# Performance work log

Hardware: AMD Instinct MI355X
Metric: run time of the kernel (lower is better)

## Reference

```python
import jax, jax.numpy as jnp
import numpy as np

D = 1024   # model dim (hard-coded in ClsNet)
H = 16     # num_heads
HD = D // H
FF = 2048  # torch TransformerEncoderLayer default dim_feedforward
B, LX, LY = 8, 512, 512
EPS = 1e-5
NEG = -1e9


def setup_inputs() -> dict:
    key = jax.random.key(0)
    ks = jax.random.split(key, 16)
    s = 0.02
    inp = {
        "x": jax.random.normal(ks[0], (B, LX, D), jnp.float32),
        "y": jax.random.normal(ks[1], (B, LY, D), jnp.float32),
        "cls": jax.random.normal(ks[2], (D,), jnp.float32) * s,
        "sep": jax.random.normal(ks[3], (D,), jnp.float32) * s,
        "px": jax.random.normal(ks[4], (D,), jnp.float32) * s,
        "py": jax.random.normal(ks[5], (D,), jnp.float32) * s,
        "Wqkv": jax.random.normal(ks[6], (3 * D, D), jnp.float32) * s,
        "bqkv": jnp.zeros((3 * D,), jnp.float32),
        "Wo": jax.random.normal(ks[7], (D, D), jnp.float32) * s,
        "bo": jnp.zeros((D,), jnp.float32),
        "W1": jax.random.normal(ks[8], (FF, D), jnp.float32) * s,
        "b1": jnp.zeros((FF,), jnp.float32),
        "W2": jax.random.normal(ks[9], (D, FF), jnp.float32) * s,
        "b2": jnp.zeros((D,), jnp.float32),
        "ln1_g": jnp.ones((D,), jnp.float32),
        "ln1_b": jnp.zeros((D,), jnp.float32),
        "ln2_g": jnp.ones((D,), jnp.float32),
        "ln2_b": jnp.zeros((D,), jnp.float32),
        "x_len": jax.random.randint(ks[10], (B,), 1, LX + 1, jnp.int32),
        "y_len": jax.random.randint(ks[11], (B,), 1, LY + 1, jnp.int32),
    }
    return inp


def _merge(x, y, cls, sep, px, py, x_len, y_len):
    # Vectorized version of ClsNet.merge: [CLS] x_i+px ... [SEP] y_i+py ... [SEP] pad...
    Bn, Lx, Dd = x.shape
    Ly = y.shape[1]
    S = Lx + Ly + 3
    pos = jnp.arange(S)[None, :]            # [1,S]
    lx = x_len[:, None]                     # [B,1]
    ly = y_len[:, None]
    is_cls = pos == 0                       # [1,S]
    is_x = (pos >= 1) & (pos <= lx)         # [B,S]
    is_sep1 = pos == lx + 1
    is_y = (pos >= lx + 2) & (pos <= lx + ly + 1)
    is_sep2 = pos == lx + ly + 2
    xi = jnp.clip(pos - 1, 0, Lx - 1)       # [1,S]
    yi = jnp.clip(pos - lx - 2, 0, Ly - 1)  # [B,S]
    xg = jnp.take_along_axis(x, xi[:, :, None], axis=1)  # [B,S,D] (broadcast batch)
    yg = jnp.take_along_axis(y, yi[:, :, None], axis=1)  # [B,S,D]
    seq = (jnp.where(is_x[..., None], xg + px, 0.0)
           + jnp.where(is_y[..., None], yg + py, 0.0)
           + is_cls[..., None] * cls
           + (is_sep1 | is_sep2)[..., None] * sep)       # [B,S,D]
    mask = is_cls | is_x | is_sep1 | is_y | is_sep2      # [B,S] True = valid token
    return seq, mask


def _ln(h, g, b):
    m = jnp.mean(h, axis=-1, keepdims=True)
    v = jnp.mean(jnp.square(h - m), axis=-1, keepdims=True)
    return (h - m) * jax.lax.rsqrt(v + EPS) * g + b


def _encoder_layer(seq, mask, Wqkv, bqkv, Wo, bo, W1, b1, W2, b2, ln1_g, ln1_b, ln2_g, ln2_b):
    Bn, S, Dd = seq.shape
    qkv = seq @ Wqkv.T + bqkv                              # [B,S,3D]
    q, k, v = jnp.split(qkv, 3, axis=-1)
    q = q.reshape(Bn, S, H, HD)
    k = k.reshape(Bn, S, H, HD)
    v = v.reshape(Bn, S, H, HD)
    bias = jnp.where(mask, 0.0, NEG)[:, None, None, :]     # padded KEYS masked out
    scores = jnp.einsum("bqhd,bkhd->bhqk", q, k) / np.sqrt(HD) + bias
    attn = jax.nn.softmax(scores, axis=-1)
    o = jnp.einsum("bhqk,bkhd->bqhd", attn, v).reshape(Bn, S, Dd)
    o = o @ Wo.T + bo
    h = _ln(seq + o, ln1_g, ln1_b)                          # post-norm (torch default)
    f = jax.nn.relu(h @ W1.T + b1) @ W2.T + b2
    return _ln(h + f, ln2_g, ln2_b)


def reference(x, y, cls, sep, px, py, Wqkv, bqkv, Wo, bo, W1, b1, W2, b2,
              ln1_g, ln1_b, ln2_g, ln2_b, x_len, y_len):
    seq, mask = _merge(x, y, cls, sep, px, py, x_len, y_len)
    out = _encoder_layer(seq, mask, Wqkv, bqkv, Wo, bo, W1, b1, W2, b2,
                         ln1_g, ln1_b, ln2_g, ln2_b)
    # torch code returns a[0] of the seq-first tensor -> the CLS position for all batches
    return out[:, 0, :]
```

## Files before the change

### kernel.cpp

```cpp
#include <hip/hip_runtime.h>
#include <hip/hip_bf16.h>

#define D_ 1024
#define H_ 16
#define FF_ 2048
#define B_ 8
#define S_ 1027
#define MPAD_ 8320
#define PSTR_ 1056
#define EPS_ 1e-5f

typedef __hip_bfloat16 bf16;
typedef unsigned short u16;
typedef unsigned int u32;
typedef __attribute__((ext_vector_type(4))) float floatx4;
typedef __bf16 bf16x8 __attribute__((ext_vector_type(8)));

__device__ __forceinline__ float2 bfpair(u32 u) {
  union { u32 u; float f; } lo, hi;
  lo.u = u << 16; hi.u = u & 0xffff0000u;
  return make_float2(lo.f, hi.f);
}

__device__ __forceinline__ u32 f2bfbits(float f) {
  union { bf16 h; u16 u; } cv; cv.h = __float2bfloat16(f); return (u32)cv.u;
}

__device__ __forceinline__ float block_sum(float x, float* red) {
  const int t = threadIdx.x;
  __syncthreads();
  red[t] = x;
  __syncthreads();
  for (int s = 128; s > 0; s >>= 1) {
    if (t < s) red[t] += red[t + s];
    __syncthreads();
  }
  return red[0];
}

__device__ __forceinline__ float block_max(float x, float* red) {
  const int t = threadIdx.x;
  __syncthreads();
  red[t] = x;
  __syncthreads();
  for (int s = 128; s > 0; s >>= 1) {
    if (t < s) red[t] = fmaxf(red[t], red[t + s]);
    __syncthreads();
  }
  return red[0];
}

__global__ void __launch_bounds__(256) build_seq_kernel(
    const float* __restrict__ x, const float* __restrict__ y,
    const float* __restrict__ cls, const float* __restrict__ sep,
    const float* __restrict__ px, const float* __restrict__ py,
    const int* __restrict__ x_len, const int* __restrict__ y_len,
    bf16* __restrict__ seq) {
  const int m = blockIdx.x, t = threadIdx.x;
  const int b = m / S_;
  const int s = m - b * S_;
  if (b >= B_) return;
  const float* src = nullptr;
  const float* add = nullptr;
  const int lx = x_len[b], ly = y_len[b];
  if (s == 0) src = cls;
  else if (s <= lx) { src = x + ((size_t)b * 512 + (s - 1)) * D_; add = px; }
  else if (s == lx + 1) src = sep;
  else if (s <= lx + ly + 1) { src = y + ((size_t)b * 512 + (s - lx - 2)) * D_; add = py; }
  else if (s == lx + ly + 2) src = sep;
  if (!src) return;
  float4 sv = ((const float4*)src)[t];
  if (add) {
    float4 av = ((const float4*)add)[t];
    sv.x += av.x; sv.y += av.y; sv.z += av.z; sv.w += av.w;
  }
  uint2 o;
  o.x = f2bfbits(sv.x) | (f2bfbits(sv.y) << 16);
  o.y = f2bfbits(sv.z) | (f2bfbits(sv.w) << 16);
  ((uint2*)(seq + (size_t)m * D_))[t] = o;
}

__global__ void __launch_bounds__(256) qproj_kernel(
    const float* __restrict__ cls, const float* __restrict__ Wqkv,
    const float* __restrict__ bqkv, float* __restrict__ q0s) {
  __shared__ float cl[D_];
  const int t = threadIdx.x;
  *(float4*)&cl[t * 4] = ((const float4*)cls)[t];
  __syncthreads();
  const int w = t >> 6, l = t & 63;
  const int r = blockIdx.x * 4 + w;
  float acc = 0.f;
#pragma unroll
  for (int ch = 0; ch < 4; ++ch) {
    float4 wv = *(const float4*)(Wqkv + (size_t)r * D_ + ch * 256 + l * 4);
    const float* c4 = &cl[ch * 256 + l * 4];
    acc += wv.x * c4[0] + wv.y * c4[1] + wv.z * c4[2] + wv.w * c4[3];
  }
#pragma unroll
  for (int off = 32; off > 0; off >>= 1) acc += __shfl_down(acc, off, 64);
  if (l == 0) q0s[r] = (acc + bqkv[r]) * 0.125f;
}

__global__ void __launch_bounds__(256) rproj_kernel(
    const float* __restrict__ Wqkv, const float* __restrict__ q0s,
    u16* __restrict__ RT_hi, u16* __restrict__ RT_lo) {
  const int h = blockIdx.y, cc = blockIdx.x, t = threadIdx.x;
  __shared__ float qs[64];
  if (t < 64) qs[t] = q0s[h * 64 + t];
  __syncthreads();
  const int c = cc * 256 + t;
  const float* Wk = Wqkv + (size_t)(D_ + h * 64) * D_ + c;
  float acc = 0.f;
#pragma unroll 8
  for (int e = 0; e < 64; ++e) acc += Wk[(size_t)e * D_] * qs[e];
  const u32 hb = f2bfbits(acc);
  union { u32 u; float f; } hv; hv.u = hb << 16;
  RT_hi[h * D_ + c] = (u16)hb;
  RT_lo[h * D_ + c] = (u16)f2bfbits(acc - hv.f);
}

__global__ void __launch_bounds__(256) scores_kernel(
    const bf16* __restrict__ seq, const u16* __restrict__ RT_hi,
    const u16* __restrict__ RT_lo, const int* __restrict__ x_len,
    const int* __restrict__ y_len, float* __restrict__ S) {
  const int m0 = blockIdx.x * 64;
  bool valid = false;
#pragma unroll
  for (int b = 0; b < B_; ++b) {
    int rs = b * S_, re = rs + x_len[b] + y_len[b] + 3;
    if (m0 < re && m0 + 64 > rs) valid = true;
  }
  if (!valid) return;
  const int t = threadIdx.x;
  const int w = t >> 6, lane = t & 63, lane16 = lane & 15, quad = lane >> 4;
  const int row = m0 + w * 16 + lane16;
  const u16* arow = (const u16*)seq + (size_t)row * D_ + quad * 8;
  const u16* bh = RT_hi + lane16 * D_ + quad * 8;
  const u16* bl = RT_lo + lane16 * D_ + quad * 8;
  floatx4 acc = {};
#pragma unroll 4
  for (int kt = 0; kt < 32; ++kt) {
    bf16x8 a  = *(const bf16x8*)(arow + kt * 32);
    bf16x8 vh = *(const bf16x8*)(bh + kt * 32);
    bf16x8 vl = *(const bf16x8*)(bl + kt * 32);
    acc = __builtin_amdgcn_mfma_f32_16x16x32_bf16(a, vh, acc, 0, 0, 0);
    acc = __builtin_amdgcn_mfma_f32_16x16x32_bf16(a, vl, acc, 0, 0, 0);
  }
  *(floatx4*)&S[(size_t)lane16 * MPAD_ + m0 + w * 16 + quad * 4] = acc;
}

__global__ void __launch_bounds__(256) softmax_kernel(
    const float* __restrict__ S, const int* __restrict__ x_len,
    const int* __restrict__ y_len, u16* __restrict__ P) {
  const int h = blockIdx.x, b = blockIdx.y, t = threadIdx.x;
  const int n = x_len[b] + y_len[b] + 3;
  __shared__ float sc[PSTR_];
  __shared__ float red[256];
  const float* Sp = S + (size_t)h * MPAD_ + b * S_;
  float lmax = -3.0e38f;
  for (int k = t; k < n; k += 256) {
    float s = Sp[k];
    sc[k] = s;
    lmax = fmaxf(lmax, s);
  }
  const float gmax = block_max(lmax, red);
  float lsum = 0.f;
  for (int k = t; k < n; k += 256) {
    float p = __expf(sc[k] - gmax);
    sc[k] = p;
    lsum += p;
  }
  const float inv = 1.0f / block_sum(lsum, red);
  u16* Pp = P + (size_t)(h * 8 + b) * PSTR_;
  for (int k = t; k < PSTR_; k += 256)
    Pp[k] = (k < n) ? (u16)f2bfbits(sc[k] * inv) : (u16)0;
}

__global__ void __launch_bounds__(256) cbar_kernel(
    const bf16* __restrict__ seq, const u16* __restrict__ P,
    const int* __restrict__ x_len, const int* __restrict__ y_len,
    float* __restrict__ cbar) {
  const int ct = blockIdx.x, b = blockIdx.y, t = threadIdx.x;
  const int c0 = ct * 64;
  const int n = x_len[b] + y_len[b] + 3;
  const int nkt = (n + 31) >> 5;
  __shared__ u16 tile[32 * 68];
  const int w = t >> 6, lane = t & 63, lane16 = lane & 15, quad = lane >> 4;
  const int sk = t >> 3, scg = (t & 7) * 8;
  floatx4 acc = {};
  for (int kt = 0; kt < nkt; ++kt) {
    const int k0 = kt * 32;
    __syncthreads();
    uint4 v = make_uint4(0u, 0u, 0u, 0u);
    if (k0 + sk < n)
      v = *(const uint4*)((const u16*)seq + (size_t)(b * S_ + k0 + sk) * D_ + c0 + scg);
    *(uint2*)&tile[sk * 68 + scg]     = make_uint2(v.x, v.y);
    *(uint2*)&tile[sk * 68 + scg + 4] = make_uint2(v.z, v.w);
    __syncthreads();
    bf16x8 a = *(const bf16x8*)(P + (size_t)(lane16 * 8 + b) * PSTR_ + k0 + quad * 8);
    union { bf16x8 v; u16 u[8]; } bu;
#pragma unroll
    for (int j = 0; j < 8; ++j)
      bu.u[j] = tile[(quad * 8 + j) * 68 + w * 16 + lane16];
    acc = __builtin_amdgcn_mfma_f32_16x16x32_bf16(a, bu.v, acc, 0, 0, 0);
  }
#pragma unroll
  for (int r = 0; r < 4; ++r)
    cbar[(size_t)(b * 16 + quad * 4 + r) * D_ + c0 + w * 16 + lane16] = acc[r];
}

template <int K, int N, int BSTR, bool INBF, bool OUTBF, bool RELU, bool PERHEAD>
__global__ void __launch_bounds__(256) gemv8_kernel(
    const void* __restrict__ in_, const float* __restrict__ W,
    const float* __restrict__ bias, void* __restrict__ out_) {
  const int t = threadIdx.x;
  const int hoff = PERHEAD ? ((blockIdx.x * 4) >> 6) * D_ : 0;
  __shared__ u16 lsb[INBF ? 8 * K : 1];
  __shared__ float lsf[INBF ? 1 : 8 * K];
  if (INBF) {
    const u16* in = (const u16*)in_;
    const int per = 8 * K / (256 * 8);
#pragma unroll
    for (int i = 0; i < per; ++i) {
      int flat = (t + i * 256) * 8;
      int b = flat / K, k = flat % K;
      *(uint4*)&lsb[flat] = *(const uint4*)(in + (size_t)b * BSTR + hoff + k);
    }
  } else {
    const float* in = (const float*)in_;
    const int per = 8 * K / (256 * 4);
#pragma unroll
    for (int i = 0; i < per; ++i) {
      int flat = (t + i * 256) * 4;
      int b = flat / K, k = flat % K;
      *(float4*)&lsf[flat] = *(const float4*)(in + (size_t)b * BSTR + hoff + k);
    }
  }
  __syncthreads();
  const int w = t >> 6, l = t & 63;
  const int r = blockIdx.x * 4 + w;
  float acc[8] = {};
#pragma unroll
  for (int ch = 0; ch < K / 256; ++ch) {
    float4 wv = *(const float4*)(W + (size_t)r * K + ch * 256 + l * 4);
#pragma unroll
    for (int b = 0; b < 8; ++b) {
      float i0, i1, i2, i3;
      if (INBF) {
        uint2 u = *(const uint2*)&lsb[b * K + ch * 256 + l * 4];
        float2 p0 = bfpair(u.x), p1 = bfpair(u.y);
        i0 = p0.x; i1 = p0.y; i2 = p1.x; i3 = p1.y;
      } else {
        const float* p = &lsf[b * K + ch * 256 + l * 4];
        i0 = p[0]; i1 = p[1]; i2 = p[2]; i3 = p[3];
      }
      acc[b] += wv.x * i0 + wv.y * i1 + wv.z * i2 + wv.w * i3;
    }
  }
#pragma unroll
  for (int off = 32; off > 0; off >>= 1)
#pragma unroll
    for (int b = 0; b < 8; ++b) acc[b] += __shfl_down(acc[b], off, 64);
  if (l == 0) {
    const float bs = bias[r];
#pragma unroll
    for (int b = 0; b < 8; ++b) {
      float v = acc[b] + bs;
      if (RELU) v = fmaxf(v, 0.f);
      if (OUTBF) ((bf16*)out_)[(size_t)b * N + r] = __float2bfloat16(v);
      else       ((float*)out_)[(size_t)b * N + r] = v;
    }
  }
}

template <bool SECOND>
__global__ void __launch_bounds__(256) ln_kernel(
    const float* __restrict__ cls, const float* __restrict__ a,
    const float* __restrict__ bvec, const float* __restrict__ g,
    const float* __restrict__ be, float* __restrict__ out) {
  const int b = blockIdx.x, t = threadIdx.x;
  __shared__ float v[D_];
  __shared__ float red[256];
  for (int i = t; i < D_; i += 256) {
    float val;
    if (SECOND) val = a[b * D_ + i] + bvec[b * D_ + i];
    else        val = cls[i] + a[b * D_ + i];
    v[i] = val;
  }
  __syncthreads();
  float ls = 0.f;
  for (int i = t; i < D_; i += 256) ls += v[i];
  const float mean = block_sum(ls, red) * (1.f / D_);
  float lv = 0.f;
  for (int i = t; i < D_; i += 256) { float dk = v[i] - mean; lv += dk * dk; }
  const float var = block_sum(lv, red) * (1.f / D_);
  const float rs = rsqrtf(var + EPS_);
  for (int i = t; i < D_; i += 256)
    out[b * D_ + i] = (v[i] - mean) * rs * g[i] + be[i];
}

extern "C" void kernel_launch(void* const* d_in, const int* in_sizes, int n_in,
                              void* d_out, int out_size, void* d_ws, size_t ws_size,
                              hipStream_t stream) {
  (void)in_sizes; (void)n_in; (void)out_size; (void)ws_size;
  const float* x    = (const float*)d_in[0];
  const float* y    = (const float*)d_in[1];
  const float* cls  = (const float*)d_in[2];
  const float* sep  = (const float*)d_in[3];
  const float* px   = (const float*)d_in[4];
  const float* py   = (const float*)d_in[5];
  const float* Wqkv = (const float*)d_in[6];
  const float* bqkv = (const float*)d_in[7];
  const float* Wo   = (const float*)d_in[8];
  const float* bo   = (const float*)d_in[9];
  const float* W1   = (const float*)d_in[10];
  const float* b1   = (const float*)d_in[11];
  const float* W2   = (const float*)d_in[12];
  const float* b2   = (const float*)d_in[13];
  const float* g1   = (const float*)d_in[14];
  const float* be1  = (const float*)d_in[15];
  const float* g2   = (const float*)d_in[16];
  const float* be2  = (const float*)d_in[17];
  const int* xl     = (const int*)d_in[18];
  const int* yl     = (const int*)d_in[19];

  char* ws = (char*)d_ws;
  bf16*  seq   = (bf16*)(ws);
  float* q0s   = (float*)(ws + 17039360);
  u16*   RT_hi = (u16*)(ws + 17043456);
  u16*   RT_lo = (u16*)(ws + 17076224);
  float* S     = (float*)(ws + 17108992);
  u16*   P     = (u16*)(ws + 17641472);
  float* cbar  = (float*)(ws + 17911808);
  float* o0    = (float*)(ws + 18436096);
  float* att   = (float*)(ws + 18468864);
  float* h0    = (float*)(ws + 18501632);
  bf16*  f1    = (bf16*)(ws + 18534400);
  float* f2    = (float*)(ws + 18567168);

  build_seq_kernel<<<MPAD_, 256, 0, stream>>>(x, y, cls, sep, px, py, xl, yl, seq);
  qproj_kernel<<<256, 256, 0, stream>>>(cls, Wqkv, bqkv, q0s);
  rproj_kernel<<<dim3(4, 16), 256, 0, stream>>>(Wqkv, q0s, RT_hi, RT_lo);
  scores_kernel<<<130, 256, 0, stream>>>(seq, RT_hi, RT_lo, xl, yl, S);
  softmax_kernel<<<dim3(16, 8), 256, 0, stream>>>(S, xl, yl, P);
  cbar_kernel<<<dim3(16, 8), 256, 0, stream>>>(seq, P, xl, yl, cbar);
  gemv8_kernel<1024, 1024, 16384, false, false, false, true>
      <<<256, 256, 0, stream>>>(cbar, Wqkv + (size_t)2048 * 1024, bqkv + 2048, o0);
  gemv8_kernel<1024, 1024, 1024, false, false, false, false>
      <<<256, 256, 0, stream>>>(o0, Wo, bo, att);
  ln_kernel<false><<<B_, 256, 0, stream>>>(cls, att, nullptr, g1, be1, h0);
  gemv8_kernel<1024, 2048, 1024, false, true, true, false>
      <<<512, 256, 0, stream>>>(h0, W1, b1, f1);
  gemv8_kernel<2048, 1024, 2048, true, false, false, false>
      <<<256, 256, 0, stream>>>(f1, W2, b2, f2);
  ln_kernel<true><<<B_, 256, 0, stream>>>(nullptr, h0, f2, g2, be2, (float*)d_out);
}
```

Baseline: 194.5 us.

## Fuse sequence merge into scores/cbar and fuse LayerNorms into neighbouring kernels

```diff
diff --git a/kernel.cpp b/kernel.cpp
--- a/kernel.cpp
+++ b/kernel.cpp
@@ -7,7 +7,7 @@
 #define B_ 8
 #define S_ 1027
 #define MPAD_ 8320
-#define PSTR_ 1056
+#define PSTR_ 1088
 #define EPS_ 1e-5f
 
 typedef __hip_bfloat16 bf16;
@@ -50,63 +50,45 @@
   return red[0];
 }
 
-__global__ void __launch_bounds__(256) build_seq_kernel(
+__device__ __forceinline__ void merge_src(
+    int b, int s, int lx, int ly,
     const float* __restrict__ x, const float* __restrict__ y,
     const float* __restrict__ cls, const float* __restrict__ sep,
     const float* __restrict__ px, const float* __restrict__ py,
-    const int* __restrict__ x_len, const int* __restrict__ y_len,
-    bf16* __restrict__ seq) {
-  const int m = blockIdx.x, t = threadIdx.x;
-  const int b = m / S_;
-  const int s = m - b * S_;
-  if (b >= B_) return;
-  const float* src = nullptr;
-  const float* add = nullptr;
-  const int lx = x_len[b], ly = y_len[b];
+    const float*& src, const float*& add) {
+  src = nullptr; add = nullptr;
   if (s == 0) src = cls;
   else if (s <= lx) { src = x + ((size_t)b * 512 + (s - 1)) * D_; add = px; }
   else if (s == lx + 1) src = sep;
   else if (s <= lx + ly + 1) { src = y + ((size_t)b * 512 + (s - lx - 2)) * D_; add = py; }
   else if (s == lx + ly + 2) src = sep;
-  if (!src) return;
-  float4 sv = ((const float4*)src)[t];
-  if (add) {
-    float4 av = ((const float4*)add)[t];
-    sv.x += av.x; sv.y += av.y; sv.z += av.z; sv.w += av.w;
-  }
-  uint2 o;
-  o.x = f2bfbits(sv.x) | (f2bfbits(sv.y) << 16);
-  o.y = f2bfbits(sv.z) | (f2bfbits(sv.w) << 16);
-  ((uint2*)(seq + (size_t)m * D_))[t] = o;
-}
-
-__global__ void __launch_bounds__(256) qproj_kernel(
+}
+
+__global__ void __launch_bounds__(256) qr_kernel(
     const float* __restrict__ cls, const float* __restrict__ Wqkv,
-    const float* __restrict__ bqkv, float* __restrict__ q0s) {
-  __shared__ float cl[D_];
-  const int t = threadIdx.x;
-  *(float4*)&cl[t * 4] = ((const float4*)cls)[t];
+    const float* __restrict__ bqkv, u16* __restrict__ RT_hi,
+    u16* __restrict__ RT_lo) {
+  const int cc = blockIdx.x, h = blockIdx.y, t = threadIdx.x;
+  __shared__ float clds[D_];
+  __shared__ float qs[64];
+  *(float4*)&clds[t * 4] = ((const float4*)cls)[t];
   __syncthreads();
   const int w = t >> 6, l = t & 63;
-  const int r = blockIdx.x * 4 + w;
-  float acc = 0.f;
-#pragma unroll
-  for (int ch = 0; ch < 4; ++ch) {
-    float4 wv = *(const float4*)(Wqkv + (size_t)r * D_ + ch * 256 + l * 4);
-    const float* c4 = &cl[ch * 256 + l * 4];
-    acc += wv.x * c4[0] + wv.y * c4[1] + wv.z * c4[2] + wv.w * c4[3];
-  }
-#pragma unroll
-  for (int off = 32; off > 0; off >>= 1) acc += __shfl_down(acc, off, 64);
-  if (l == 0) q0s[r] = (acc + bqkv[r]) * 0.125f;
-}
-
-__global__ void __launch_bounds__(256) rproj_kernel(
-    const float* __restrict__ Wqkv, const float* __restrict__ q0s,
-    u16* __restrict__ RT_hi, u16* __restrict__ RT_lo) {
-  const int h = blockIdx.y, cc = blockIdx.x, t = threadIdx.x;
-  __shared__ float qs[64];
-  if (t < 64) qs[t] = q0s[h * 64 + t];
+#pragma unroll 2
+  for (int e8 = 0; e8 < 16; ++e8) {
+    const int e = e8 * 4 + w;
+    const float4* wr = (const float4*)(Wqkv + (size_t)(h * 64 + e) * D_) + l;
+    float acc = 0.f;
+#pragma unroll
+    for (int c = 0; c < 4; ++c) {
+      float4 wv = wr[c * 64];
+      const float* cp = &clds[c * 256 + l * 4];
+      acc += wv.x * cp[0] + wv.y * cp[1] + wv.z * cp[2] + wv.w * cp[3];
+    }
+#pragma unroll
+    for (int off = 32; off > 0; off >>= 1) acc += __shfl_down(acc, off, 64);
+    if (l == 0) qs[e] = (acc + bqkv[h * 64 + e]) * 0.125f;
+  }
   __syncthreads();
   const int c = cc * 256 + t;
   const float* Wk = Wqkv + (size_t)(D_ + h * 64) * D_ + c;
@@ -120,31 +102,56 @@
 }
 
 __global__ void __launch_bounds__(256) scores_kernel(
-    const bf16* __restrict__ seq, const u16* __restrict__ RT_hi,
-    const u16* __restrict__ RT_lo, const int* __restrict__ x_len,
-    const int* __restrict__ y_len, float* __restrict__ S) {
+    const float* __restrict__ x, const float* __restrict__ y,
+    const float* __restrict__ cls, const float* __restrict__ sep,
+    const float* __restrict__ px, const float* __restrict__ py,
+    const int* __restrict__ x_len, const int* __restrict__ y_len,
+    const u16* __restrict__ RT_hi, const u16* __restrict__ RT_lo,
+    float* __restrict__ S) {
   const int m0 = blockIdx.x * 64;
-  bool valid = false;
+  bool anyvalid = false;
 #pragma unroll
   for (int b = 0; b < B_; ++b) {
     int rs = b * S_, re = rs + x_len[b] + y_len[b] + 3;
-    if (m0 < re && m0 + 64 > rs) valid = true;
-  }
-  if (!valid) return;
+    if (m0 < re && m0 + 64 > rs) anyvalid = true;
+  }
+  if (!anyvalid) return;
   const int t = threadIdx.x;
   const int w = t >> 6, lane = t & 63, lane16 = lane & 15, quad = lane >> 4;
   const int row = m0 + w * 16 + lane16;
-  const u16* arow = (const u16*)seq + (size_t)row * D_ + quad * 8;
+  const int b = row / S_;
+  const int s = row - b * S_;
+  const float* src = nullptr;
+  const float* add = nullptr;
+  if (b < B_) merge_src(b, s, x_len[b], y_len[b], x, y, cls, sep, px, py, src, add);
   const u16* bh = RT_hi + lane16 * D_ + quad * 8;
   const u16* bl = RT_lo + lane16 * D_ + quad * 8;
   floatx4 acc = {};
 #pragma unroll 4
   for (int kt = 0; kt < 32; ++kt) {
-    bf16x8 a  = *(const bf16x8*)(arow + kt * 32);
+    const int col = kt * 32 + quad * 8;
+    union { bf16x8 v; u16 u[8]; } au;
+    if (src) {
+      float4 a0 = *(const float4*)(src + col);
+      float4 a1 = *(const float4*)(src + col + 4);
+      if (add) {
+        float4 p0 = *(const float4*)(add + col);
+        float4 p1 = *(const float4*)(add + col + 4);
+        a0.x += p0.x; a0.y += p0.y; a0.z += p0.z; a0.w += p0.w;
+        a1.x += p1.x; a1.y += p1.y; a1.z += p1.z; a1.w += p1.w;
+      }
+      au.u[0] = (u16)f2bfbits(a0.x); au.u[1] = (u16)f2bfbits(a0.y);
+      au.u[2] = (u16)f2bfbits(a0.z); au.u[3] = (u16)f2bfbits(a0.w);
+      au.u[4] = (u16)f2bfbits(a1.x); au.u[5] = (u16)f2bfbits(a1.y);
+      au.u[6] = (u16)f2bfbits(a1.z); au.u[7] = (u16)f2bfbits(a1.w);
+    } else {
+#pragma unroll
+      for (int j = 0; j < 8; ++j) au.u[j] = 0;
+    }
     bf16x8 vh = *(const bf16x8*)(bh + kt * 32);
     bf16x8 vl = *(const bf16x8*)(bl + kt * 32);
-    acc = __builtin_amdgcn_mfma_f32_16x16x32_bf16(a, vh, acc, 0, 0, 0);
-    acc = __builtin_amdgcn_mfma_f32_16x16x32_bf16(a, vl, acc, 0, 0, 0);
+    acc = __builtin_amdgcn_mfma_f32_16x16x32_bf16(au.v, vh, acc, 0, 0, 0);
+    acc = __builtin_amdgcn_mfma_f32_16x16x32_bf16(au.v, vl, acc, 0, 0, 0);
   }
   *(floatx4*)&S[(size_t)lane16 * MPAD_ + m0 + w * 16 + quad * 4] = acc;
 }
@@ -177,36 +184,60 @@
 }
 
 __global__ void __launch_bounds__(256) cbar_kernel(
-    const bf16* __restrict__ seq, const u16* __restrict__ P,
+    const float* __restrict__ x, const float* __restrict__ y,
+    const float* __restrict__ cls, const float* __restrict__ sep,
+    const float* __restrict__ px, const float* __restrict__ py,
     const int* __restrict__ x_len, const int* __restrict__ y_len,
-    float* __restrict__ cbar) {
+    const u16* __restrict__ P, float* __restrict__ cbar) {
   const int ct = blockIdx.x, b = blockIdx.y, t = threadIdx.x;
   const int c0 = ct * 64;
-  const int n = x_len[b] + y_len[b] + 3;
-  const int nkt = (n + 31) >> 5;
-  __shared__ u16 tile[32 * 68];
+  const int lx = x_len[b], ly = y_len[b];
+  const int n = lx + ly + 3;
+  const int nkt = (n + 63) >> 6;
+  __shared__ u16 tile[64 * 70];
   const int w = t >> 6, lane = t & 63, lane16 = lane & 15, quad = lane >> 4;
-  const int sk = t >> 3, scg = (t & 7) * 8;
+  const int r = t >> 2;
+  const int g = (t & 3) * 16;
+  const u16* Pp = P + (size_t)(lane16 * 8 + b) * PSTR_;
   floatx4 acc = {};
   for (int kt = 0; kt < nkt; ++kt) {
-    const int k0 = kt * 32;
+    const int k0 = kt * 64;
     __syncthreads();
-    uint4 v = make_uint4(0u, 0u, 0u, 0u);
-    if (k0 + sk < n)
-      v = *(const uint4*)((const u16*)seq + (size_t)(b * S_ + k0 + sk) * D_ + c0 + scg);
-    *(uint2*)&tile[sk * 68 + scg]     = make_uint2(v.x, v.y);
-    *(uint2*)&tile[sk * 68 + scg + 4] = make_uint2(v.z, v.w);
+    const int gk = k0 + r;
+    u32 packed[8] = {};
+    if (gk < n) {
+      const float* src; const float* add;
+      merge_src(b, gk, lx, ly, x, y, cls, sep, px, py, src, add);
+      const float* sp = src + c0 + g;
+#pragma unroll
+      for (int q = 0; q < 4; ++q) {
+        float4 v = *(const float4*)(sp + q * 4);
+        if (add) {
+          float4 a = *(const float4*)(add + c0 + g + q * 4);
+          v.x += a.x; v.y += a.y; v.z += a.z; v.w += a.w;
+        }
+        packed[q * 2]     = f2bfbits(v.x) | (f2bfbits(v.y) << 16);
+        packed[q * 2 + 1] = f2bfbits(v.z) | (f2bfbits(v.w) << 16);
+      }
+    }
+#pragma unroll
+    for (int q = 0; q < 8; ++q)
+      *(u32*)&tile[r * 70 + g + q * 2] = packed[q];
     __syncthreads();
-    bf16x8 a = *(const bf16x8*)(P + (size_t)(lane16 * 8 + b) * PSTR_ + k0 + quad * 8);
-    union { bf16x8 v; u16 u[8]; } bu;
-#pragma unroll
-    for (int j = 0; j < 8; ++j)
-      bu.u[j] = tile[(quad * 8 + j) * 68 + w * 16 + lane16];
-    acc = __builtin_amdgcn_mfma_f32_16x16x32_bf16(a, bu.v, acc, 0, 0, 0);
-  }
-#pragma unroll
-  for (int r = 0; r < 4; ++r)
-    cbar[(size_t)(b * 16 + quad * 4 + r) * D_ + c0 + w * 16 + lane16] = acc[r];
+#pragma unroll
+    for (int half = 0; half < 2; ++half) {
+      const int kk = half * 32;
+      bf16x8 a = *(const bf16x8*)(Pp + k0 + kk + quad * 8);
+      union { bf16x8 v; u16 u[8]; } bu;
+#pragma unroll
+      for (int j = 0; j < 8; ++j)
+        bu.u[j] = tile[(kk + quad * 8 + j) * 70 + w * 16 + lane16];
+      acc = __builtin_amdgcn_mfma_f32_16x16x32_bf16(a, bu.v, acc, 0, 0, 0);
+    }
+  }
+#pragma unroll
+  for (int r4 = 0; r4 < 4; ++r4)
+    cbar[(size_t)(b * 16 + quad * 4 + r4) * D_ + c0 + w * 16 + lane16] = acc[r4];
 }
 
 template <int K, int N, int BSTR, bool INBF, bool OUTBF, bool RELU, bool PERHEAD>
@@ -273,30 +304,103 @@
   }
 }
 
-template <bool SECOND>
-__global__ void __launch_bounds__(256) ln_kernel(
-    const float* __restrict__ cls, const float* __restrict__ a,
-    const float* __restrict__ bvec, const float* __restrict__ g,
-    const float* __restrict__ be, float* __restrict__ out) {
+__global__ void __launch_bounds__(256) w1ln_kernel(
+    const float* __restrict__ att, const float* __restrict__ cls,
+    const float* __restrict__ g1, const float* __restrict__ be1,
+    const float* __restrict__ W1, const float* __restrict__ b1,
+    bf16* __restrict__ f1) {
+  const int t = threadIdx.x;
+  __shared__ float ls[8 * D_];
+  __shared__ float mn[8], rsd[8];
+  float4 cv = ((const float4*)cls)[t];
+#pragma unroll
+  for (int i = 0; i < 8; ++i) {
+    float4 a = ((const float4*)(att + (size_t)i * D_))[t];
+    a.x += cv.x; a.y += cv.y; a.z += cv.z; a.w += cv.w;
+    *(float4*)&ls[i * D_ + t * 4] = a;
+  }
+  __syncthreads();
+  {
+    const int b = t >> 5, j = t & 31;
+    const float* base = &ls[b * D_ + j * 32];
+    float s = 0.f, s2 = 0.f;
+#pragma unroll
+    for (int k = 0; k < 32; ++k) { float v = base[k]; s += v; s2 += v * v; }
+#pragma unroll
+    for (int off = 16; off > 0; off >>= 1) {
+      s += __shfl_down(s, off, 32);
+      s2 += __shfl_down(s2, off, 32);
+    }
+    if (j == 0) {
+      float mean = s * (1.f / D_);
+      mn[b] = mean;
+      rsd[b] = rsqrtf(s2 * (1.f / D_) - mean * mean + EPS_);
+    }
+  }
+  __syncthreads();
+  {
+    const int b = t >> 5, j = t & 31;
+    const float mean = mn[b], rs = rsd[b];
+    float* base = &ls[b * D_ + j * 32];
+    const float* gp = &g1[j * 32];
+    const float* bp = &be1[j * 32];
+#pragma unroll
+    for (int k = 0; k < 32; ++k)
+      base[k] = (base[k] - mean) * rs * gp[k] + bp[k];
+  }
+  __syncthreads();
+  const int w = t >> 6, l = t & 63;
+  const int r = blockIdx.x * 4 + w;
+  float acc[8] = {};
+#pragma unroll
+  for (int ch = 0; ch < 4; ++ch) {
+    float4 wv = *(const float4*)(W1 + (size_t)r * D_ + ch * 256 + l * 4);
+#pragma unroll
+    for (int b = 0; b < 8; ++b) {
+      const float* p = &ls[b * D_ + ch * 256 + l * 4];
+      acc[b] += wv.x * p[0] + wv.y * p[1] + wv.z * p[2] + wv.w * p[3];
+    }
+  }
+#pragma unroll
+  for (int off = 32; off > 0; off >>= 1)
+#pragma unroll
+    for (int b = 0; b < 8; ++b) acc[b] += __shfl_down(acc[b], off, 64);
+  if (l == 0) {
+    const float bs = b1[r];
+#pragma unroll
+    for (int b = 0; b < 8; ++b)
+      f1[(size_t)b * FF_ + r] = __float2bfloat16(fmaxf(acc[b] + bs, 0.f));
+  }
+}
+
+__global__ void __launch_bounds__(256) ln2_kernel(
+    const float* __restrict__ cls, const float* __restrict__ att,
+    const float* __restrict__ f2, const float* __restrict__ g1,
+    const float* __restrict__ be1, const float* __restrict__ g2,
+    const float* __restrict__ be2, float* __restrict__ out) {
   const int b = blockIdx.x, t = threadIdx.x;
   __shared__ float v[D_];
   __shared__ float red[256];
-  for (int i = t; i < D_; i += 256) {
-    float val;
-    if (SECOND) val = a[b * D_ + i] + bvec[b * D_ + i];
-    else        val = cls[i] + a[b * D_ + i];
-    v[i] = val;
-  }
+  for (int i = t; i < D_; i += 256) v[i] = cls[i] + att[(size_t)b * D_ + i];
   __syncthreads();
   float ls = 0.f;
   for (int i = t; i < D_; i += 256) ls += v[i];
-  const float mean = block_sum(ls, red) * (1.f / D_);
+  const float m1 = block_sum(ls, red) * (1.f / D_);
   float lv = 0.f;
-  for (int i = t; i < D_; i += 256) { float dk = v[i] - mean; lv += dk * dk; }
-  const float var = block_sum(lv, red) * (1.f / D_);
-  const float rs = rsqrtf(var + EPS_);
+  for (int i = t; i < D_; i += 256) { float dk = v[i] - m1; lv += dk * dk; }
+  const float rs1 = rsqrtf(block_sum(lv, red) * (1.f / D_) + EPS_);
+  __syncthreads();
   for (int i = t; i < D_; i += 256)
-    out[b * D_ + i] = (v[i] - mean) * rs * g[i] + be[i];
+    v[i] = (v[i] - m1) * rs1 * g1[i] + be1[i] + f2[(size_t)b * D_ + i];
+  __syncthreads();
+  float ls2 = 0.f;
+  for (int i = t; i < D_; i += 256) ls2 += v[i];
+  const float m2 = block_sum(ls2, red) * (1.f / D_);
+  float lv2 = 0.f;
+  for (int i = t; i < D_; i += 256) { float dk = v[i] - m2; lv2 += dk * dk; }
+  const float rs2 = rsqrtf(block_sum(lv2, red) * (1.f / D_) + EPS_);
+  for (int i = t; i < D_; i += 256)
+    out[(size_t)b * D_ + i] = (v[i] - m2) * rs2 * g2[i] + be2[i];
 }
 
 extern "C" void kernel_launch(void* const* d_in, const int* in_sizes, int n_in,
@@ -325,33 +429,29 @@
   const int* yl     = (const int*)d_in[19];
 
   char* ws = (char*)d_ws;
-  bf16*  seq   = (bf16*)(ws);
-  float* q0s   = (float*)(ws + 17039360);
-  u16*   RT_hi = (u16*)(ws + 17043456);
-  u16*   RT_lo = (u16*)(ws + 17076224);
-  float* S     = (float*)(ws + 17108992);
-  u16*   P     = (u16*)(ws + 17641472);
-  float* cbar  = (float*)(ws + 17911808);
-  float* o0    = (float*)(ws + 18436096);
-  float* att   = (float*)(ws + 18468864);
-  float* h0    = (float*)(ws + 18501632);
-  bf16*  f1    = (bf16*)(ws + 18534400);
-  float* f2    = (float*)(ws + 18567168);
-
-  build_seq_kernel<<<MPAD_, 256, 0, stream>>>(x, y, cls, sep, px, py, xl, yl, seq);
-  qproj_kernel<<<256, 256, 0, stream>>>(cls, Wqkv, bqkv, q0s);
-  rproj_kernel<<<dim3(4, 16), 256, 0, stream>>>(Wqkv, q0s, RT_hi, RT_lo);
-  scores_kernel<<<130, 256, 0, stream>>>(seq, RT_hi, RT_lo, xl, yl, S);
+  u16*   RT_hi = (u16*)(ws);
+  u16*   RT_lo = (u16*)(ws + 32768);
+  float* S     = (float*)(ws + 65536);
+  u16*   P     = (u16*)(ws + 598016);
+  float* cbar  = (float*)(ws + 876544);
+  float* o0    = (float*)(ws + 1400832);
+  float* att   = (float*)(ws + 1433600);
+  bf16*  f1    = (bf16*)(ws + 1466368);
+  float* f2    = (float*)(ws + 1499136);
+
+  qr_kernel<<<dim3(4, 16), 256, 0, stream>>>(cls, Wqkv, bqkv, RT_hi, RT_lo);
+  scores_kernel<<<130, 256, 0, stream>>>(x, y, cls, sep, px, py, xl, yl,
+                                         RT_hi, RT_lo, S);
   softmax_kernel<<<dim3(16, 8), 256, 0, stream>>>(S, xl, yl, P);
-  cbar_kernel<<<dim3(16, 8), 256, 0, stream>>>(seq, P, xl, yl, cbar);
+  cbar_kernel<<<dim3(16, 8), 256, 0, stream>>>(x, y, cls, sep, px, py, xl, yl,
+                                               P, cbar);
   gemv8_kernel<1024, 1024, 16384, false, false, false, true>
       <<<256, 256, 0, stream>>>(cbar, Wqkv + (size_t)2048 * 1024, bqkv + 2048, o0);
   gemv8_kernel<1024, 1024, 1024, false, false, false, false>
       <<<256, 256, 0, stream>>>(o0, Wo, bo, att);
-  ln_kernel<false><<<B_, 256, 0, stream>>>(cls, att, nullptr, g1, be1, h0);
-  gemv8_kernel<1024, 2048, 1024, false, true, true, false>
-      <<<512, 256, 0, stream>>>(h0, W1, b1, f1);
+  w1ln_kernel<<<512, 256, 0, stream>>>(att, cls, g1, be1, W1, b1, f1);
   gemv8_kernel<2048, 1024, 2048, true, false, false, false>
       <<<256, 256, 0, stream>>>(f1, W2, b2, f2);
-  ln_kernel<true><<<B_, 256, 0, stream>>>(nullptr, h0, f2, g2, be2, (float*)d_out);
-}
+  ln2_kernel<<<B_, 256, 0, stream>>>(cls, att, f2, g1, be1, g2, be2,
+                                     (float*)d_out);
+}
```

Result: slower. 230.7 us (+18.6%).
